# Kernel optimization log

Hardware: AMD Instinct MI355X
Metric: run time of the kernel (lower is better)

Reference implementation:

```python
import jax, jax.numpy as jnp
import numpy as np

# Dims: batch=2, seqlen=L=384, d_inner=d=384, d_state=s=384, dt_rank=r=384, d_conv=4.
# NOTE: the original torch module only runs when L == d_inner == d_state == dt_rank
# (see its broadcasting in SelectiveScan and the Linear layer plumbing); we reproduce
# that exact (quirky) broadcast faithfully.
B_, L_, D_, S_, R_, K_ = 2, 384, 384, 384, 384, 4


def setup_inputs() -> dict:
    key = jax.random.key(0)
    ks = jax.random.split(key, 9)
    f32 = jnp.float32
    return {
        "x": jax.random.normal(ks[0], (B_, L_, D_), f32),
        "A_log": jax.random.normal(ks[1], (D_, S_), f32) * 0.02,
        "D": jax.random.normal(ks[2], (D_,), f32) * 0.02,
        "dt_w": jax.random.normal(ks[3], (D_, R_), f32) * 0.02,
        "dt_b": jax.random.normal(ks[4], (D_,), f32) * 0.02,
        "B_w": jax.random.normal(ks[5], (S_, D_), f32) * (1.0 / np.sqrt(D_)),
        "C_w": jax.random.normal(ks[6], (S_, D_), f32) * (1.0 / np.sqrt(D_)),
        "conv_w": jax.random.normal(ks[7], (D_, 1, K_), f32) * (1.0 / np.sqrt(K_)),
        "conv_b": jnp.zeros((D_,), f32),
    }


def _forward(x, A_log, D, dt_w, dt_b, B_w, C_w, conv_w, conv_b):
    b, L, d = x.shape
    A = -jnp.exp(A_log)                       # (d, s)
    dt = jax.nn.softplus(x @ dt_w.T + dt_b)   # (b, L, d)
    x_dbl = x @ B_w.T                         # (b, L, s)
    Bm = x_dbl @ B_w.T                        # (b, L, s)  (module applies B_proj twice)
    Cm = x_dbl @ C_w.T                        # (b, L, s)
    # causal depthwise conv1d: pad (k-1) on the left == torch pad k-1 then [:, :, :L]
    xc = jax.lax.conv_general_dilated(
        x.transpose(0, 2, 1), conv_w, (1,), [(conv_w.shape[-1] - 1, 0)],
        feature_group_count=d, dimension_numbers=("NCH", "OIH", "NCH"))
    xc = xc + conv_b[None, :, None]
    u = jax.nn.silu(xc.transpose(0, 2, 1))    # (b, L, d)
    # selective scan (faithful to the torch SelectiveScan broadcasting)
    deltaA = jnp.exp(dt[..., None] * A[None, None])          # (b, L, d, s)
    deltaB_u = dt[..., None] * Bm[:, None, :, :] * u[..., None]  # (b, L, d, s), needs L==d

    def step(h, inp):
        dA_i, dBu_i, C_i, u_i = inp
        h = dA_i * h + dBu_i                  # (b, d, s)
        y = jnp.sum(h * C_i[:, None, :], -1) + u_i * D  # (b, d)
        return h, y

    h0 = jnp.zeros((b, d, deltaA.shape[-1]), x.dtype)
    xs = (deltaA.transpose(1, 0, 2, 3), deltaB_u.transpose(1, 0, 2, 3),
          Cm.transpose(1, 0, 2), u.transpose(1, 0, 2))
    _, ys = jax.lax.scan(step, h0, xs)        # ys: (L, b, d)
    return ys.transpose(1, 0, 2)


def reference(x, A_log, D, dt_w, dt_b, B_w, C_w, conv_w, conv_b):
    return _forward(x, A_log, D, dt_w, dt_b, B_w, C_w, conv_w, conv_b)
```

## Files before the change

### kernel.cpp

```cpp
#include <hip/hip_runtime.h>
#include <math.h>

#define B_SZ 2
#define L_SZ 384
#define D_SZ 384
#define S_SZ 384
#define BLK_ELEMS (L_SZ * D_SZ)
#define TOT_ELEMS (B_SZ * L_SZ * D_SZ)
#define LOG2E 1.4426950408889634f

typedef __attribute__((ext_vector_type(8))) short bf16x8;
typedef __attribute__((ext_vector_type(4))) float f32x4;
typedef __attribute__((ext_vector_type(2))) unsigned int u32x2;

__device__ __forceinline__ float fexp2(float x) {
  return __builtin_amdgcn_exp2f(x);
}
__device__ __forceinline__ float softplus_f(float z) {
  return (z > 20.f) ? z : log1pf(__expf(z));
}
__device__ __forceinline__ unsigned short f2bf(float f) {
  unsigned int u = __float_as_uint(f);
  return (unsigned short)((u + 0x7FFFu + ((u >> 16) & 1u)) >> 16);
}
#define PIPELINE_FENCE() asm volatile("" ::: "memory")

__device__ __forceinline__ bf16x8 cvt8(const float* p) {
  const f32x4 v0 = *(const f32x4*)p;
  const f32x4 v1 = *(const f32x4*)(p + 4);
  union { unsigned int u[4]; bf16x8 v; } r;
  asm("v_cvt_pk_bf16_f32 %0, %1, %2" : "=v"(r.u[0]) : "v"(v0[0]), "v"(v0[1]));
  asm("v_cvt_pk_bf16_f32 %0, %1, %2" : "=v"(r.u[1]) : "v"(v0[2]), "v"(v0[3]));
  asm("v_cvt_pk_bf16_f32 %0, %1, %2" : "=v"(r.u[2]) : "v"(v1[0]), "v"(v1[1]));
  asm("v_cvt_pk_bf16_f32 %0, %1, %2" : "=v"(r.u[3]) : "v"(v1[2]), "v"(v1[3]));
  return r.v;
}

template <int CTRL>
__device__ __forceinline__ float dpp_mov(float v) {
  return __int_as_float(
      __builtin_amdgcn_update_dpp(0, __float_as_int(v), CTRL, 0xF, 0xF, true));
}

__device__ __forceinline__ float fold_xor16(float r) {
#if __has_builtin(__builtin_amdgcn_permlane16_swap)
  const unsigned ru = __float_as_uint(r);
  u32x2 p = __builtin_amdgcn_permlane16_swap(ru, ru, false, false);
  return __uint_as_float(p[0]) + __uint_as_float(p[1]);
#else
  return r + __shfl_xor(r, 16, 64);
#endif
}
__device__ __forceinline__ float fold_xor32(float r) {
#if __has_builtin(__builtin_amdgcn_permlane32_swap)
  const unsigned ru = __float_as_uint(r);
  u32x2 p = __builtin_amdgcn_permlane32_swap(ru, ru, false, false);
  return __uint_as_float(p[0]) + __uint_as_float(p[1]);
#else
  return r + __shfl_xor(r, 32, 64);
#endif
}

template <int MODE>
__global__ __launch_bounds__(128, 2) void mfma_dual_gemm(
    const void* __restrict__ Av, const float* __restrict__ W1,
    const float* __restrict__ W2, const float* __restrict__ bias,
    float* __restrict__ O1, void* __restrict__ O2v) {
  __shared__ unsigned short sA[32 * 392];
  __shared__ unsigned short sW1[16 * 392];
  __shared__ unsigned short sW2[16 * 392];

  const int t = threadIdx.x;
  const int wv = t >> 6;
  const int lane = t & 63;
  const int nt = blockIdx.x;
  const int mrow = blockIdx.y;

  const float* W1b = W1 + nt * 16 * 384;
  const float* W2b = W2 + nt * 16 * 384;

  if constexpr (MODE == 1) {
    const float* Ab = (const float*)Av + mrow * 32 * 384;
#pragma unroll
    for (int it = 0; it < 12; ++it) {
      const int id = t + it * 128;
      const int row = id / 48, col = id - row * 48;
      *(bf16x8*)&sA[row * 392 + col * 8] = cvt8(Ab + id * 8);
    }
  } else {
    const unsigned short* Ab = (const unsigned short*)Av + mrow * 32 * 384;
#pragma unroll
    for (int it = 0; it < 12; ++it) {
      const int id = t + it * 128;
      const int row = id / 48, col = id - row * 48;
      *(bf16x8*)&sA[row * 392 + col * 8] = *(const bf16x8*)(Ab + id * 8);
    }
  }
#pragma unroll
  for (int it = 0; it < 6; ++it) {
    const int id = t + it * 128;
    const int row = id / 48, col = id - row * 48;
    *(bf16x8*)&sW1[row * 392 + col * 8] = cvt8(W1b + id * 8);
    *(bf16x8*)&sW2[row * 392 + col * 8] = cvt8(W2b + id * 8);
  }
  __syncthreads();

  const int rc = lane & 15;
  const int quad = lane >> 4;
  bf16x8 af[12], w1f[12], w2f[12];
#pragma unroll
  for (int kt = 0; kt < 12; ++kt) {
    af[kt] = *(const bf16x8*)&sA[(wv * 16 + rc) * 392 + quad * 8 + kt * 32];
    w1f[kt] = *(const bf16x8*)&sW1[rc * 392 + quad * 8 + kt * 32];
    w2f[kt] = *(const bf16x8*)&sW2[rc * 392 + quad * 8 + kt * 32];
  }
  PIPELINE_FENCE();
  f32x4 acc1 = {0.f, 0.f, 0.f, 0.f};
  f32x4 acc2 = {0.f, 0.f, 0.f, 0.f};
#pragma unroll
  for (int kt = 0; kt < 12; ++kt) {
    acc1 = __builtin_amdgcn_mfma_f32_16x16x32_bf16(af[kt], w1f[kt], acc1, 0, 0, 0);
    acc2 = __builtin_amdgcn_mfma_f32_16x16x32_bf16(af[kt], w2f[kt], acc2, 0, 0, 0);
  }
  const int col = nt * 16 + rc;
  const int row0 = mrow * 32 + wv * 16 + quad * 4;
  if constexpr (MODE == 1) {
    unsigned short* O2 = (unsigned short*)O2v;
    const float bb = bias[col];
#pragma unroll
    for (int r = 0; r < 4; ++r) {
      O1[(row0 + r) * 384 + col] = softplus_f(acc1[r] + bb);
      O2[(row0 + r) * 384 + col] = f2bf(acc2[r]);
    }
  } else {
#pragma unroll
    for (int r = 0; r < 4; ++r)
      O1[(row0 + r) * 384 + col] = acc1[r];
    const unsigned int p01 =
        (unsigned int)f2bf(acc2[0]) | ((unsigned int)f2bf(acc2[1]) << 16);
    const unsigned int p23 =
        (unsigned int)f2bf(acc2[2]) | ((unsigned int)f2bf(acc2[3]) << 16);
    u32x2 q = {p01, p23};
    *((u32x2*)O2v + ((row0 >> 2) * 384 + col)) = q;
  }
}

__global__ __launch_bounds__(256) void conv_tr_kernel(
    const float* __restrict__ x, const float* __restrict__ cw,
    const float* __restrict__ cb, const float* __restrict__ dt,
    float* __restrict__ u, float* __restrict__ dt_t,
    float* __restrict__ dtu_t) {
  __shared__ float Tdt[32][33];
  __shared__ float Tdu[32][33];
  const int tx = threadIdx.x;
  const int ty = threadIdx.y;
  const int b = blockIdx.z;
  const int i0 = blockIdx.y * 32;
  const int l0 = blockIdx.x * 32;
  const int gi = i0 + tx;
  const float cbv = cb[gi];
  const float cw0 = cw[gi * 4 + 0], cw1 = cw[gi * 4 + 1];
  const float cw2 = cw[gi * 4 + 2], cw3 = cw[gi * 4 + 3];
#pragma unroll
  for (int r = 0; r < 4; ++r) {
    const int l = l0 + ty + 8 * r;
    float acc = cbv;
    const float x3 = x[(b * L_SZ + l) * D_SZ + gi];
    const float x2 = (l >= 1) ? x[(b * L_SZ + l - 1) * D_SZ + gi] : 0.f;
    const float x1 = (l >= 2) ? x[(b * L_SZ + l - 2) * D_SZ + gi] : 0.f;
    const float x0 = (l >= 3) ? x[(b * L_SZ + l - 3) * D_SZ + gi] : 0.f;
    acc = fmaf(x0, cw0, acc);
    acc = fmaf(x1, cw1, acc);
    acc = fmaf(x2, cw2, acc);
    acc = fmaf(x3, cw3, acc);
    const float uv = acc / (1.f + __expf(-acc));
    const int off = (b * L_SZ + l) * D_SZ + gi;
    u[off] = uv;
    const float dtv = dt[off];
    Tdt[ty + 8 * r][tx] = dtv;
    Tdu[ty + 8 * r][tx] = dtv * uv;
  }
  __syncthreads();
#pragma unroll
  for (int r = 0; r < 4; ++r) {
    const int il = ty + 8 * r;
    const int off = (b * D_SZ + i0 + il) * L_SZ + l0 + tx;
    dt_t[off] = Tdt[tx][il];
    dtu_t[off] = Tdu[tx][il];
  }
}

struct SChunk {
  f32x4 d0, d1, u0, u1;
};

#define SLOAD_CHUNK(S, SDT, SDU)                                               \
  asm volatile("s_load_dwordx4 %0, %4, 0x0\n\t"                                \
               "s_load_dwordx4 %1, %4, 0x10\n\t"                               \
               "s_load_dwordx4 %2, %5, 0x0\n\t"                                \
               "s_load_dwordx4 %3, %5, 0x10"                                   \
               : "=&s"(S.d0), "=&s"(S.d1), "=&s"(S.u0), "=&s"(S.u1)            \
               : "s"(SDT), "s"(SDU));

#define SWAIT(S)                                                               \
  asm volatile("s_waitcnt lgkmcnt(0)"                                          \
               : "+s"(S.d0), "+s"(S.d1), "+s"(S.u0), "+s"(S.u1))

#define SADV()                                                                 \
  { sdt += 8; sdu += 8; }

__global__ __launch_bounds__(64, 4) void scan_kernel(
    const float* __restrict__ A_log, const float* __restrict__ dt_t,
    const float* __restrict__ dtu_t, const float* __restrict__ Bm,
    const u32x2* __restrict__ Cmq, float* __restrict__ part) {
  const int bid = blockIdx.x;
  const int xcd = bid & 7;
  const int slot = bid >> 3;
  const int sid = xcd * 96 + slot / 6;
  const int w = slot % 6;
  const int lane = threadIdx.x;
  const int b = sid / D_SZ;
  const int i = sid % D_SZ;
  const int j = w * 64 + lane;

  const float a2 = -__expf(A_log[i * S_SZ + j]) * LOG2E;
  const float bw = Bm[(b * D_SZ + i) * S_SZ + j];
  float h = 0.f;

  const float* sdt = dt_t + (b * D_SZ + i) * L_SZ;
  const float* sdu = dtu_t + (b * D_SZ + i) * L_SZ;
  const u32x2* cq = Cmq + (b * 96) * 384 + j;

  const int sq = (((lane >> 3) & 1) << 2) | (((lane >> 2) & 1) << 1) | (lane & 1);
  const bool storer = (lane & 0x32) == 0;
  float* pstore = part + ((w * B_SZ + b) * D_SZ + i) * L_SZ + sq;

  auto compute_chunk = [&](u32x2 qa_c, u32x2 qb_c, SChunk& S) {
    float acc[8];
    const float dts[8] = {S.d0[0], S.d0[1], S.d0[2], S.d0[3],
                          S.d1[0], S.d1[1], S.d1[2], S.d1[3]};
    const float dus[8] = {S.u0[0], S.u0[1], S.u0[2], S.u0[3],
                          S.u1[0], S.u1[1], S.u1[2], S.u1[3]};
    const unsigned int qs[4] = {qa_c[0], qa_c[1], qb_c[0], qb_c[1]};
#pragma unroll
    for (int s = 0; s < 8; ++s) {
      const float e = fexp2(dts[s] * a2);
      h = fmaf(e, h, bw * dus[s]);
      const unsigned int cw32 =
          (s & 1) ? (qs[s >> 1] & 0xFFFF0000u) : (qs[s >> 1] << 16);
      acc[s] = h * __uint_as_float(cw32);
    }
    {
      const bool hi = (lane & 8) != 0;
#pragma unroll
      for (int q = 0; q < 4; ++q) {
        const float keep = hi ? acc[q + 4] : acc[q];
        const float send = hi ? acc[q] : acc[q + 4];
        acc[q] = keep + dpp_mov<0x140>(send);
      }
    }
    {
      const bool hi = (lane & 4) != 0;
#pragma unroll
      for (int q = 0; q < 2; ++q) {
        const float keep = hi ? acc[q + 2] : acc[q];
        const float send = hi ? acc[q] : acc[q + 2];
        acc[q] = keep + dpp_mov<0x141>(send);
      }
    }
    {
      const bool hi = (lane & 1) != 0;
      const float keep = hi ? acc[1] : acc[0];
      const float send = hi ? acc[0] : acc[1];
      acc[0] = keep + dpp_mov<0xB1>(send);
    }
    float r = acc[0];
    r += dpp_mov<0x4E>(r);
    r = fold_xor16(r);
    r = fold_xor32(r);
    if (storer) *pstore = r;
    pstore += 8;
  };

  SChunk S0, S1;
  u32x2 qa = cq[0], qb = cq[384];
  cq += 768;
  SLOAD_CHUNK(S0, sdt, sdu); SADV();

#define STEP(SC, SN)                                                           \
  {                                                                            \
    const u32x2 qa_n = cq[0];                                                  \
    const u32x2 qb_n = cq[384];                                                \
    cq += 768;                                                                 \
    SWAIT(SC);                                                                 \
    SLOAD_CHUNK(SN, sdt, sdu);                                                 \
    SADV();                                                                    \
    compute_chunk(qa, qb, SC);                                                 \
    qa = qa_n;                                                                 \
    qb = qb_n;                                                                 \
  }

#pragma unroll 1
  for (int it = 0; it < 8; ++it) {
    STEP(S0, S1);
    STEP(S1, S0);
    STEP(S0, S1);
    STEP(S1, S0);
    STEP(S0, S1);
    STEP(S1, S0);
  }
#undef STEP
}

__global__ __launch_bounds__(256) void combine_kernel(
    const float* __restrict__ part, const float* __restrict__ u,
    const float* __restrict__ Dv, float* __restrict__ y) {
  __shared__ float T[32][33];
  const int tx = threadIdx.x;
  const int ty0 = threadIdx.y;
  const int b = blockIdx.z;
  const int i0 = blockIdx.y * 32;
  const int l0 = blockIdx.x * 32;
#pragma unroll
  for (int r = 0; r < 4; ++r) {
    const int il = ty0 + 8 * r;
    float s = 0.f;
#pragma unroll
    for (int w = 0; w < 6; ++w)
      s += part[((w * B_SZ + b) * D_SZ + i0 + il) * L_SZ + l0 + tx];
    T[il][tx] = s;
  }
  __syncthreads();
#pragma unroll
  for (int r = 0; r < 4; ++r) {
    const int ll = ty0 + 8 * r;
    const int gi = i0 + tx;
    const int off = (b * L_SZ + l0 + ll) * D_SZ + gi;
    y[off] = fmaf(u[off], Dv[gi], T[tx][ll]);
  }
}

extern "C" void kernel_launch(void* const* d_in, const int* in_sizes, int n_in,
                              void* d_out, int out_size, void* d_ws,
                              size_t ws_size, hipStream_t stream) {
  const float* x = (const float*)d_in[0];
  const float* A_log = (const float*)d_in[1];
  const float* D = (const float*)d_in[2];
  const float* dt_w = (const float*)d_in[3];
  const float* dt_b = (const float*)d_in[4];
  const float* B_w = (const float*)d_in[5];
  const float* C_w = (const float*)d_in[6];
  const float* conv_w = (const float*)d_in[7];
  const float* conv_b = (const float*)d_in[8];
  float* y = (float*)d_out;

  float* ws = (float*)d_ws;
  float* dt = ws;
  float* u = ws + TOT_ELEMS;
  float* Bm = ws + 2 * TOT_ELEMS;
  float* dt_t = ws + 3 * TOT_ELEMS;
  float* dtu_t = ws + 4 * TOT_ELEMS;
  float* part = ws + 5 * TOT_ELEMS;
  unsigned short* bfarea = (unsigned short*)(ws + 11 * TOT_ELEMS);
  u32x2* Cmq = (u32x2*)bfarea;
  unsigned short* xdblbf = bfarea + TOT_ELEMS;

  mfma_dual_gemm<1><<<dim3(24, 24), 128, 0, stream>>>(x, dt_w, B_w, dt_b, dt, xdblbf);
  mfma_dual_gemm<2><<<dim3(24, 24), 128, 0, stream>>>(xdblbf, B_w, C_w, nullptr, Bm, Cmq);
  conv_tr_kernel<<<dim3(L_SZ / 32, D_SZ / 32, B_SZ), dim3(32, 8), 0, stream>>>(
      x, conv_w, conv_b, dt, u, dt_t, dtu_t);
  scan_kernel<<<4608, 64, 0, stream>>>(A_log, dt_t, dtu_t, Bm, Cmq, part);
  combine_kernel<<<dim3(L_SZ / 32, D_SZ / 32, B_SZ), dim3(32, 8), 0, stream>>>(
      part, u, D, y);
}
```

Baseline: 128.1 us.

## Fuse first dual GEMM with causal conv and transpose into one kernel

The first GEMM (dt projection with softplus plus the x_dbl projection) is merged with the conv/SiLU/transpose kernel. Each block now computes a 32x32 output tile, where it previously computed 32x16. The softplus dt tile stays in shared memory and is transposed directly, so the fp32 dt round-trip through global memory and one kernel launch go away. In exchange, the GEMM grid shrinks to 288 blocks, each uses more shared memory, and the K-loop no longer preloads its fragments into registers.

Result: no change. 128.1 us (+0.0%).

```diff
diff --git a/kernel.cpp b/kernel.cpp
--- a/kernel.cpp
+++ b/kernel.cpp
@@ -61,45 +61,32 @@
 #endif
 }
 
-template <int MODE>
-__global__ __launch_bounds__(128, 2) void mfma_dual_gemm(
-    const void* __restrict__ Av, const float* __restrict__ W1,
-    const float* __restrict__ W2, const float* __restrict__ bias,
-    float* __restrict__ O1, void* __restrict__ O2v) {
+__global__ __launch_bounds__(128, 2) void gemm1_conv_kernel(
+    const float* __restrict__ x, const float* __restrict__ dt_w,
+    const float* __restrict__ B_w, const float* __restrict__ dt_b,
+    const float* __restrict__ cw, const float* __restrict__ cb,
+    unsigned short* __restrict__ xdbl, float* __restrict__ u,
+    float* __restrict__ dt_t, float* __restrict__ dtu_t) {
   __shared__ unsigned short sA[32 * 392];
-  __shared__ unsigned short sW1[16 * 392];
-  __shared__ unsigned short sW2[16 * 392];
+  __shared__ unsigned short sW1[32 * 392];
+  __shared__ unsigned short sW2[32 * 392];
+  float* const Tdt = (float*)sA;
+  float* const Tdu = (float*)sA + 32 * 33;
 
   const int t = threadIdx.x;
   const int wv = t >> 6;
   const int lane = t & 63;
-  const int nt = blockIdx.x;
+  const int ip = blockIdx.x;
   const int mrow = blockIdx.y;
 
-  const float* W1b = W1 + nt * 16 * 384;
-  const float* W2b = W2 + nt * 16 * 384;
-
-  if constexpr (MODE == 1) {
-    const float* Ab = (const float*)Av + mrow * 32 * 384;
-#pragma unroll
-    for (int it = 0; it < 12; ++it) {
-      const int id = t + it * 128;
-      const int row = id / 48, col = id - row * 48;
-      *(bf16x8*)&sA[row * 392 + col * 8] = cvt8(Ab + id * 8);
-    }
-  } else {
-    const unsigned short* Ab = (const unsigned short*)Av + mrow * 32 * 384;
-#pragma unroll
-    for (int it = 0; it < 12; ++it) {
-      const int id = t + it * 128;
-      const int row = id / 48, col = id - row * 48;
-      *(bf16x8*)&sA[row * 392 + col * 8] = *(const bf16x8*)(Ab + id * 8);
-    }
-  }
-#pragma unroll
-  for (int it = 0; it < 6; ++it) {
+  const float* Ab = x + mrow * 32 * 384;
+  const float* W1b = dt_w + ip * 32 * 384;
+  const float* W2b = B_w + ip * 32 * 384;
+#pragma unroll
+  for (int it = 0; it < 12; ++it) {
     const int id = t + it * 128;
     const int row = id / 48, col = id - row * 48;
+    *(bf16x8*)&sA[row * 392 + col * 8] = cvt8(Ab + id * 8);
     *(bf16x8*)&sW1[row * 392 + col * 8] = cvt8(W1b + id * 8);
     *(bf16x8*)&sW2[row * 392 + col * 8] = cvt8(W2b + id * 8);
   }
@@ -107,63 +94,51 @@
 
   const int rc = lane & 15;
   const int quad = lane >> 4;
-  bf16x8 af[12], w1f[12], w2f[12];
+  f32x4 acc1a = {0.f, 0.f, 0.f, 0.f}, acc1b = {0.f, 0.f, 0.f, 0.f};
+  f32x4 acc2a = {0.f, 0.f, 0.f, 0.f}, acc2b = {0.f, 0.f, 0.f, 0.f};
 #pragma unroll
   for (int kt = 0; kt < 12; ++kt) {
-    af[kt] = *(const bf16x8*)&sA[(wv * 16 + rc) * 392 + quad * 8 + kt * 32];
-    w1f[kt] = *(const bf16x8*)&sW1[rc * 392 + quad * 8 + kt * 32];
-    w2f[kt] = *(const bf16x8*)&sW2[rc * 392 + quad * 8 + kt * 32];
-  }
-  PIPELINE_FENCE();
-  f32x4 acc1 = {0.f, 0.f, 0.f, 0.f};
-  f32x4 acc2 = {0.f, 0.f, 0.f, 0.f};
-#pragma unroll
-  for (int kt = 0; kt < 12; ++kt) {
-    acc1 = __builtin_amdgcn_mfma_f32_16x16x32_bf16(af[kt], w1f[kt], acc1, 0, 0, 0);
-    acc2 = __builtin_amdgcn_mfma_f32_16x16x32_bf16(af[kt], w2f[kt], acc2, 0, 0, 0);
-  }
-  const int col = nt * 16 + rc;
-  const int row0 = mrow * 32 + wv * 16 + quad * 4;
-  if constexpr (MODE == 1) {
-    unsigned short* O2 = (unsigned short*)O2v;
-    const float bb = bias[col];
-#pragma unroll
-    for (int r = 0; r < 4; ++r) {
-      O1[(row0 + r) * 384 + col] = softplus_f(acc1[r] + bb);
-      O2[(row0 + r) * 384 + col] = f2bf(acc2[r]);
-    }
-  } else {
-#pragma unroll
-    for (int r = 0; r < 4; ++r)
-      O1[(row0 + r) * 384 + col] = acc1[r];
-    const unsigned int p01 =
-        (unsigned int)f2bf(acc2[0]) | ((unsigned int)f2bf(acc2[1]) << 16);
-    const unsigned int p23 =
-        (unsigned int)f2bf(acc2[2]) | ((unsigned int)f2bf(acc2[3]) << 16);
-    u32x2 q = {p01, p23};
-    *((u32x2*)O2v + ((row0 >> 2) * 384 + col)) = q;
-  }
-}
-
-__global__ __launch_bounds__(256) void conv_tr_kernel(
-    const float* __restrict__ x, const float* __restrict__ cw,
-    const float* __restrict__ cb, const float* __restrict__ dt,
-    float* __restrict__ u, float* __restrict__ dt_t,
-    float* __restrict__ dtu_t) {
-  __shared__ float Tdt[32][33];
-  __shared__ float Tdu[32][33];
-  const int tx = threadIdx.x;
-  const int ty = threadIdx.y;
-  const int b = blockIdx.z;
-  const int i0 = blockIdx.y * 32;
-  const int l0 = blockIdx.x * 32;
+    const int ko = quad * 8 + kt * 32;
+    const bf16x8 af = *(const bf16x8*)&sA[(wv * 16 + rc) * 392 + ko];
+    const bf16x8 w1a = *(const bf16x8*)&sW1[rc * 392 + ko];
+    const bf16x8 w1b = *(const bf16x8*)&sW1[(16 + rc) * 392 + ko];
+    const bf16x8 w2a = *(const bf16x8*)&sW2[rc * 392 + ko];
+    const bf16x8 w2b = *(const bf16x8*)&sW2[(16 + rc) * 392 + ko];
+    acc1a = __builtin_amdgcn_mfma_f32_16x16x32_bf16(af, w1a, acc1a, 0, 0, 0);
+    acc1b = __builtin_amdgcn_mfma_f32_16x16x32_bf16(af, w1b, acc1b, 0, 0, 0);
+    acc2a = __builtin_amdgcn_mfma_f32_16x16x32_bf16(af, w2a, acc2a, 0, 0, 0);
+    acc2b = __builtin_amdgcn_mfma_f32_16x16x32_bf16(af, w2b, acc2b, 0, 0, 0);
+  }
+  __syncthreads();
+
+  const int lrow0 = wv * 16 + quad * 4;
+  const int grow0 = mrow * 32 + lrow0;
+  const int gcola = ip * 32 + rc;
+  const int gcolb = gcola + 16;
+  const float bba = dt_b[gcola];
+  const float bbb = dt_b[gcolb];
+#pragma unroll
+  for (int r = 0; r < 4; ++r) {
+    xdbl[(grow0 + r) * 384 + gcola] = f2bf(acc2a[r]);
+    xdbl[(grow0 + r) * 384 + gcolb] = f2bf(acc2b[r]);
+    Tdt[(lrow0 + r) * 33 + rc] = softplus_f(acc1a[r] + bba);
+    Tdt[(lrow0 + r) * 33 + rc + 16] = softplus_f(acc1b[r] + bbb);
+  }
+  __syncthreads();
+
+  const int tx = t & 31;
+  const int tyc = t >> 5;
+  const int b = mrow / 12;
+  const int l0 = (mrow % 12) * 32;
+  const int i0 = ip * 32;
   const int gi = i0 + tx;
   const float cbv = cb[gi];
   const float cw0 = cw[gi * 4 + 0], cw1 = cw[gi * 4 + 1];
   const float cw2 = cw[gi * 4 + 2], cw3 = cw[gi * 4 + 3];
 #pragma unroll
-  for (int r = 0; r < 4; ++r) {
-    const int l = l0 + ty + 8 * r;
+  for (int r = 0; r < 8; ++r) {
+    const int ll = tyc + 4 * r;
+    const int l = l0 + ll;
     float acc = cbv;
     const float x3 = x[(b * L_SZ + l) * D_SZ + gi];
     const float x2 = (l >= 1) ? x[(b * L_SZ + l - 1) * D_SZ + gi] : 0.f;
@@ -174,20 +149,80 @@
     acc = fmaf(x2, cw2, acc);
     acc = fmaf(x3, cw3, acc);
     const float uv = acc / (1.f + __expf(-acc));
-    const int off = (b * L_SZ + l) * D_SZ + gi;
-    u[off] = uv;
-    const float dtv = dt[off];
-    Tdt[ty + 8 * r][tx] = dtv;
-    Tdu[ty + 8 * r][tx] = dtv * uv;
-  }
-  __syncthreads();
-#pragma unroll
-  for (int r = 0; r < 4; ++r) {
-    const int il = ty + 8 * r;
+    u[(b * L_SZ + l) * D_SZ + gi] = uv;
+    Tdu[ll * 33 + tx] = Tdt[ll * 33 + tx] * uv;
+  }
+  __syncthreads();
+#pragma unroll
+  for (int r = 0; r < 8; ++r) {
+    const int il = tyc + 4 * r;
     const int off = (b * D_SZ + i0 + il) * L_SZ + l0 + tx;
-    dt_t[off] = Tdt[tx][il];
-    dtu_t[off] = Tdu[tx][il];
-  }
+    dt_t[off] = Tdt[tx * 33 + il];
+    dtu_t[off] = Tdu[tx * 33 + il];
+  }
+}
+
+__global__ __launch_bounds__(128, 2) void mfma_gemm2(
+    const unsigned short* __restrict__ Abf, const float* __restrict__ W1,
+    const float* __restrict__ W2, float* __restrict__ O1,
+    u32x2* __restrict__ O2q) {
+  __shared__ unsigned short sA[32 * 392];
+  __shared__ unsigned short sW1[16 * 392];
+  __shared__ unsigned short sW2[16 * 392];
+
+  const int t = threadIdx.x;
+  const int wv = t >> 6;
+  const int lane = t & 63;
+  const int nt = blockIdx.x;
+  const int mrow = blockIdx.y;
+
+  const unsigned short* Ab = Abf + mrow * 32 * 384;
+  const float* W1b = W1 + nt * 16 * 384;
+  const float* W2b = W2 + nt * 16 * 384;
+
+#pragma unroll
+  for (int it = 0; it < 12; ++it) {
+    const int id = t + it * 128;
+    const int row = id / 48, col = id - row * 48;
+    *(bf16x8*)&sA[row * 392 + col * 8] = *(const bf16x8*)(Ab + id * 8);
+  }
+#pragma unroll
+  for (int it = 0; it < 6; ++it) {
+    const int id = t + it * 128;
+    const int row = id / 48, col = id - row * 48;
+    *(bf16x8*)&sW1[row * 392 + col * 8] = cvt8(W1b + id * 8);
+    *(bf16x8*)&sW2[row * 392 + col * 8] = cvt8(W2b + id * 8);
+  }
+  __syncthreads();
+
+  const int rc = lane & 15;
+  const int quad = lane >> 4;
+  bf16x8 af[12], w1f[12], w2f[12];
+#pragma unroll
+  for (int kt = 0; kt < 12; ++kt) {
+    af[kt] = *(const bf16x8*)&sA[(wv * 16 + rc) * 392 + quad * 8 + kt * 32];
+    w1f[kt] = *(const bf16x8*)&sW1[rc * 392 + quad * 8 + kt * 32];
+    w2f[kt] = *(const bf16x8*)&sW2[rc * 392 + quad * 8 + kt * 32];
+  }
+  PIPELINE_FENCE();
+  f32x4 acc1 = {0.f, 0.f, 0.f, 0.f};
+  f32x4 acc2 = {0.f, 0.f, 0.f, 0.f};
+#pragma unroll
+  for (int kt = 0; kt < 12; ++kt) {
+    acc1 = __builtin_amdgcn_mfma_f32_16x16x32_bf16(af[kt], w1f[kt], acc1, 0, 0, 0);
+    acc2 = __builtin_amdgcn_mfma_f32_16x16x32_bf16(af[kt], w2f[kt], acc2, 0, 0, 0);
+  }
+  const int col = nt * 16 + rc;
+  const int row0 = mrow * 32 + wv * 16 + quad * 4;
+#pragma unroll
+  for (int r = 0; r < 4; ++r)
+    O1[(row0 + r) * 384 + col] = acc1[r];
+  const unsigned int p01 =
+      (unsigned int)f2bf(acc2[0]) | ((unsigned int)f2bf(acc2[1]) << 16);
+  const unsigned int p23 =
+      (unsigned int)f2bf(acc2[2]) | ((unsigned int)f2bf(acc2[3]) << 16);
+  u32x2 q = {p01, p23};
+  O2q[(row0 >> 2) * 384 + col] = q;
 }
 
 struct SChunk {
@@ -355,20 +390,18 @@
   float* y = (float*)d_out;
 
   float* ws = (float*)d_ws;
-  float* dt = ws;
-  float* u = ws + TOT_ELEMS;
-  float* Bm = ws + 2 * TOT_ELEMS;
-  float* dt_t = ws + 3 * TOT_ELEMS;
-  float* dtu_t = ws + 4 * TOT_ELEMS;
-  float* part = ws + 5 * TOT_ELEMS;
-  unsigned short* bfarea = (unsigned short*)(ws + 11 * TOT_ELEMS);
+  float* u = ws;
+  float* Bm = ws + TOT_ELEMS;
+  float* dt_t = ws + 2 * TOT_ELEMS;
+  float* dtu_t = ws + 3 * TOT_ELEMS;
+  float* part = ws + 4 * TOT_ELEMS;
+  unsigned short* bfarea = (unsigned short*)(ws + 10 * TOT_ELEMS);
   u32x2* Cmq = (u32x2*)bfarea;
   unsigned short* xdblbf = bfarea + TOT_ELEMS;
 
-  mfma_dual_gemm<1><<<dim3(24, 24), 128, 0, stream>>>(x, dt_w, B_w, dt_b, dt, xdblbf);
-  mfma_dual_gemm<2><<<dim3(24, 24), 128, 0, stream>>>(xdblbf, B_w, C_w, nullptr, Bm, Cmq);
-  conv_tr_kernel<<<dim3(L_SZ / 32, D_SZ / 32, B_SZ), dim3(32, 8), 0, stream>>>(
-      x, conv_w, conv_b, dt, u, dt_t, dtu_t);
+  gemm1_conv_kernel<<<dim3(12, 24), 128, 0, stream>>>(
+      x, dt_w, B_w, dt_b, conv_w, conv_b, xdblbf, u, dt_t, dtu_t);
+  mfma_gemm2<<<dim3(24, 24), 128, 0, stream>>>(xdblbf, B_w, C_w, Bm, Cmq);
   scan_kernel<<<4608, 64, 0, stream>>>(A_log, dt_t, dtu_t, Bm, Cmq, part);
   combine_kernel<<<dim3(L_SZ / 32, D_SZ / 32, B_SZ), dim3(32, 8), 0, stream>>>(
       part, u, D, y);
```
